# Performance work log

Hardware: AMD Instinct MI355X
Metric: run time of the kernel (lower is better)

## Reference

```python
import jax, jax.numpy as jnp
import numpy as np

N = 50000        # nodes
DEG = 16         # avg degree
E_RAND = N * DEG # random directed edges (before self-loops)
B = 4
F_IN = 64
F_OUT = 64


def _build_normalized_adjacency():
    """COO form of A_hat = D^{-1/2} (A + I) D^{-1/2} for a random sparse graph."""
    rng = np.random.default_rng(0)
    src = rng.integers(0, N, size=E_RAND)
    dst = rng.integers(0, N, size=E_RAND)
    rows = np.concatenate([src, np.arange(N)])  # add self-loops (A + I)
    cols = np.concatenate([dst, np.arange(N)])
    d = np.bincount(rows, minlength=N).astype(np.float32)  # row sums of A_tilde
    d_inv_sqrt = np.where(d > 0, 1.0 / np.sqrt(d), 0.0).astype(np.float32)
    vals = d_inv_sqrt[rows] * d_inv_sqrt[cols]
    return rows.astype(np.int32), cols.astype(np.int32), vals


def setup_inputs() -> dict:
    key = jax.random.key(0)
    k1, k2 = jax.random.split(key, 2)
    rows, cols, vals = _build_normalized_adjacency()
    x = jax.random.normal(k1, (B, N, F_IN), dtype=jnp.float32)
    # trunc_normal_(std=0.1) approximated by scaled normal
    weight = jax.random.normal(k2, (F_IN, F_OUT), dtype=jnp.float32) * 0.1
    bias = jnp.full((F_OUT,), 0.1, dtype=jnp.float32)
    return {
        "x": x,
        "vals": jnp.asarray(vals),
        "weight": weight,
        "bias": bias,
        "rows": jnp.asarray(rows),
        "cols": jnp.asarray(cols),
    }


def reference(x, vals, weight, bias, rows, cols):
    # SpMM: agg[b, r, f] = sum_e vals[e] * x[b, cols[e], f], scattered to rows[e]
    contrib = x[:, cols, :] * vals[None, :, None]          # [B, E, F_in]
    agg = jax.ops.segment_sum(contrib.transpose(1, 0, 2),  # [E, B, F_in]
                              rows, num_segments=N)        # [N, B, F_in]
    agg = agg.transpose(1, 0, 2)                           # [B, N, F_in]
    out = jnp.einsum('bnf,fo->bno', agg, weight) + bias    # dense GEMM + bias
    return jax.nn.elu(out)
```

## Files before the change

### kernel.cpp

```cpp
#include <hip/hip_runtime.h>
#include <math.h>

#define NNODES 50000
#define BB 4
#define FF 64
#define CAP 64

#define TROWS 64
#define GEMM_NB ((BB * NNODES) / TROWS)
#define RPB 4

typedef _Float16 f16;
typedef __attribute__((ext_vector_type(8))) _Float16 f16x8;
typedef __attribute__((ext_vector_type(4))) float f32x4;


__device__ inline unsigned short f2bf(float f) {
    unsigned u = __float_as_uint(f);
    u += 0x7fffu + ((u >> 16) & 1u);
    return (unsigned short)(u >> 16);
}

__device__ inline void bf4fma(float v, uint2 hv, float& a0, float& a1, float& a2, float& a3) {
    a0 = fmaf(v, __uint_as_float(hv.x << 16),         a0);
    a1 = fmaf(v, __uint_as_float(hv.x & 0xffff0000u), a1);
    a2 = fmaf(v, __uint_as_float(hv.y << 16),         a2);
    a3 = fmaf(v, __uint_as_float(hv.y & 0xffff0000u), a3);
}


__global__ __launch_bounds__(256) void prep_kernel(const int* __restrict__ rows,
                                                   const int* __restrict__ cols,
                                                   const float* __restrict__ vals,
                                                   int* __restrict__ cnt,
                                                   unsigned* __restrict__ edata, int ES,
                                                   int cstride,
                                                   const float* __restrict__ x,
                                                   const float* __restrict__ w,
                                                   unsigned short* __restrict__ h) {
    __shared__ f16 xs[64][72];
    __shared__ f16 wt[64][72];
    int t = threadIdx.x;
    long rowBase = (long)blockIdx.x * TROWS;

    int e = blockIdx.x * 256 + t;
    bool has_e = (e < ES);
    int r_e = 0, c_e = 0;
    float v_e = 0.f;
    if (has_e) { r_e = rows[e]; c_e = cols[e]; v_e = vals[e]; }

    #pragma unroll
    for (int i = 0; i < 4; ++i) {
        int s = t + i * 256;
        int r = s >> 4, c4 = s & 15;
        const float4* xp = (const float4*)(x + (rowBase + r) * 64 + c4 * 4);
        float4 xv;
        xv.x = __builtin_nontemporal_load(&xp->x);
        xv.y = __builtin_nontemporal_load(&xp->y);
        xv.z = __builtin_nontemporal_load(&xp->z);
        xv.w = __builtin_nontemporal_load(&xp->w);
        xs[r][c4 * 4 + 0] = (f16)xv.x;
        xs[r][c4 * 4 + 1] = (f16)xv.y;
        xs[r][c4 * 4 + 2] = (f16)xv.z;
        xs[r][c4 * 4 + 3] = (f16)xv.w;
        float4 wv = *(const float4*)(w + r * 64 + c4 * 4);
        wt[c4 * 4 + 0][r] = (f16)wv.x;
        wt[c4 * 4 + 1][r] = (f16)wv.y;
        wt[c4 * 4 + 2][r] = (f16)wv.z;
        wt[c4 * 4 + 3][r] = (f16)wv.w;
    }
    __syncthreads();

    int wid = t >> 6, l = t & 63;
    int arow = (wid << 4) + (l & 15);
    int kg   = (l >> 4) << 3;
    f16x8 aLo = *(const f16x8*)&xs[arow][kg];
    f16x8 aHi = *(const f16x8*)&xs[arow][32 + kg];
    f32x4 acc[4] = {{0.f,0.f,0.f,0.f},{0.f,0.f,0.f,0.f},{0.f,0.f,0.f,0.f},{0.f,0.f,0.f,0.f}};
    #pragma unroll
    for (int c = 0; c < 4; ++c) {
        f16x8 bLo = *(const f16x8*)&wt[c * 16 + (l & 15)][kg];
        f16x8 bHi = *(const f16x8*)&wt[c * 16 + (l & 15)][32 + kg];
        acc[c] = __builtin_amdgcn_mfma_f32_16x16x32_f16(aLo, bLo, acc[c], 0, 0, 0);
        acc[c] = __builtin_amdgcn_mfma_f32_16x16x32_f16(aHi, bHi, acc[c], 0, 0, 0);
    }

    int mloc = (l >> 4) << 2, fcol = l & 15;
    #pragma unroll
    for (int reg = 0; reg < 4; ++reg) {
        long m = rowBase + (wid << 4) + mloc + reg;
        int  b = (int)(m / NNODES);
        int  n = (int)(m - (long)b * NNODES);
        unsigned short* hp = h + ((size_t)n * BB + b) * 64 + fcol;
        #pragma unroll
        for (int c = 0; c < 4; ++c) hp[c * 16] = f2bf(acc[c][reg]);
    }

    if (has_e) {
        int pos = atomicAdd(&cnt[(size_t)r_e * cstride], 1);
        if (pos < CAP) {
            unsigned p = ((unsigned)f2bf(v_e) << 16) | (unsigned)c_e;
            edata[(size_t)r_e * CAP + pos] = p;
        }
    }
}


__global__ __launch_bounds__(256) void gather_kernel(const unsigned short* __restrict__ h,
                                                     const int* __restrict__ cnt,
                                                     const unsigned* __restrict__ edata,
                                                     const float* __restrict__ vals,
                                                     const float* __restrict__ bias,
                                                     float* __restrict__ out,
                                                     int cstride, int ES) {
    int wave = threadIdx.x >> 6;
    int lane = threadIdx.x & 63;
    int r = blockIdx.x * RPB + wave;
    if (r >= NNODES) return;
    int deg = cnt[(size_t)r * cstride];
    if (deg > CAP) deg = CAP;
    int b  = lane >> 4;
    int fq = lane & 15;
    const unsigned short* hb = h + b * 64 + fq * 4;
    unsigned my_p = 0u;
    if (lane < deg) {
        const unsigned* ep = &edata[(size_t)r * CAP + lane];
        my_p = __builtin_nontemporal_load(ep);
    }
    float vs = vals[ES + r];
    uint2 hs = *(const uint2*)(hb + (size_t)r * 256);
    float4 b4 = ((const float4*)bias)[fq];

    float a0 = 0.f, a1 = 0.f, a2 = 0.f, a3 = 0.f;
    int dg8 = (deg + 7) & ~7;
    for (int k = 0; k < dg8; k += 8) {
        unsigned p0 = __shfl(my_p, k,     64), p1 = __shfl(my_p, k + 1, 64);
        unsigned p2 = __shfl(my_p, k + 2, 64), p3 = __shfl(my_p, k + 3, 64);
        unsigned p4 = __shfl(my_p, k + 4, 64), p5 = __shfl(my_p, k + 5, 64);
        unsigned p6 = __shfl(my_p, k + 6, 64), p7 = __shfl(my_p, k + 7, 64);
        uint2 h0 = *(const uint2*)(hb + (size_t)(p0 & 0xFFFFu) * 256);
        uint2 h1 = *(const uint2*)(hb + (size_t)(p1 & 0xFFFFu) * 256);
        uint2 h2 = *(const uint2*)(hb + (size_t)(p2 & 0xFFFFu) * 256);
        uint2 h3 = *(const uint2*)(hb + (size_t)(p3 & 0xFFFFu) * 256);
        uint2 h4 = *(const uint2*)(hb + (size_t)(p4 & 0xFFFFu) * 256);
        uint2 h5 = *(const uint2*)(hb + (size_t)(p5 & 0xFFFFu) * 256);
        uint2 h6 = *(const uint2*)(hb + (size_t)(p6 & 0xFFFFu) * 256);
        uint2 h7 = *(const uint2*)(hb + (size_t)(p7 & 0xFFFFu) * 256);
        bf4fma(__uint_as_float(p0 & 0xFFFF0000u), h0, a0, a1, a2, a3);
        bf4fma(__uint_as_float(p1 & 0xFFFF0000u), h1, a0, a1, a2, a3);
        bf4fma(__uint_as_float(p2 & 0xFFFF0000u), h2, a0, a1, a2, a3);
        bf4fma(__uint_as_float(p3 & 0xFFFF0000u), h3, a0, a1, a2, a3);
        bf4fma(__uint_as_float(p4 & 0xFFFF0000u), h4, a0, a1, a2, a3);
        bf4fma(__uint_as_float(p5 & 0xFFFF0000u), h5, a0, a1, a2, a3);
        bf4fma(__uint_as_float(p6 & 0xFFFF0000u), h6, a0, a1, a2, a3);
        bf4fma(__uint_as_float(p7 & 0xFFFF0000u), h7, a0, a1, a2, a3);
    }
    bf4fma(vs, hs, a0, a1, a2, a3);
    a0 += b4.x; a1 += b4.y; a2 += b4.z; a3 += b4.w;
    a0 = a0 > 0.f ? a0 : expm1f(a0);
    a1 = a1 > 0.f ? a1 : expm1f(a1);
    a2 = a2 > 0.f ? a2 : expm1f(a2);
    a3 = a3 > 0.f ? a3 : expm1f(a3);
    float4 o = make_float4(a0, a1, a2, a3);
    *(float4*)(out + ((size_t)b * NNODES + r) * 64 + fq * 4) = o;
}


static inline size_t align256(size_t x) { return (x + 255) & ~(size_t)255; }

extern "C" void kernel_launch(void* const* d_in, const int* in_sizes, int n_in,
                              void* d_out, int out_size, void* d_ws, size_t ws_size,
                              hipStream_t stream) {
    const float* x    = (const float*)d_in[0];
    const float* vals = (const float*)d_in[1];
    const float* w    = (const float*)d_in[2];
    const float* bias = (const float*)d_in[3];
    const int*   rows = (const int*)d_in[4];
    const int*   cols = (const int*)d_in[5];
    float* out = (float*)d_out;
    const int E  = in_sizes[1];
    const int ES = E - NNODES;

    size_t h_b     = align256((size_t)BB * NNODES * FF * sizeof(unsigned short));
    size_t edata_b = align256((size_t)NNODES * CAP * sizeof(unsigned));
    int cstride = 16;
    if (h_b + edata_b + align256((size_t)NNODES * 16 * sizeof(int)) > ws_size) cstride = 1;

    char* ws = (char*)d_ws;
    size_t off = 0;
    unsigned short* h = (unsigned short*)(ws + off);  off += h_b;
    int* cnt = (int*)(ws + off);
    off += align256((size_t)NNODES * cstride * sizeof(int));
    unsigned* edata = (unsigned*)(ws + off);          off += edata_b;

    hipMemsetAsync(cnt, 0, (size_t)NNODES * cstride * sizeof(int), stream);
    prep_kernel<<<GEMM_NB, 256, 0, stream>>>(rows, cols, vals, cnt, edata, ES, cstride, x, w, h);
    gather_kernel<<<(NNODES + RPB - 1) / RPB, 256, 0, stream>>>(h, cnt, edata, vals, bias, out, cstride, ES);
}
```

Baseline: 133.2 us.

## Precompute transposed f16 weights once and load GEMM operands directly into registers

A new init kernel zeroes the count array (replacing hipMemsetAsync) and writes a transposed f16 copy of the weight matrix once. The prep kernel then drops its shared-memory staging and __syncthreads, loading x rows straight into MFMA operand registers and reading the pre-transposed weights from global memory. It also swaps the MFMA operand order so each lane holds four consecutive output features, which lets h be stored as ushort4 vectors instead of scalar shorts. In exchange, x is read with strided 32-byte per-lane accesses rather than fully coalesced rows, and weight reads now hit L2 from every block.

Measured after the change: 130.4 us. 2.1% less time.

```diff
diff --git a/kernel.cpp b/kernel.cpp
--- a/kernel.cpp
+++ b/kernel.cpp
@@ -11,6 +11,7 @@
 #define RPB 4
 
 typedef _Float16 f16;
+typedef __attribute__((ext_vector_type(4))) _Float16 f16x4;
 typedef __attribute__((ext_vector_type(8))) _Float16 f16x8;
 typedef __attribute__((ext_vector_type(4))) float f32x4;
 
@@ -26,6 +27,23 @@
     a1 = fmaf(v, __uint_as_float(hv.x & 0xffff0000u), a1);
     a2 = fmaf(v, __uint_as_float(hv.y << 16),         a2);
     a3 = fmaf(v, __uint_as_float(hv.y & 0xffff0000u), a3);
+}
+
+
+__global__ __launch_bounds__(256) void init_kernel(int* __restrict__ cnt, int n4,
+                                                   const float* __restrict__ w,
+                                                   f16* __restrict__ wt) {
+    int i = blockIdx.x * 256 + threadIdx.x;
+    if (i < n4) ((int4*)cnt)[i] = make_int4(0, 0, 0, 0);
+    if (i < 1024) {
+        int f = i >> 4, k0 = (i & 15) << 2;
+        f16x4 v;
+        v[0] = (f16)w[(k0 + 0) * 64 + f];
+        v[1] = (f16)w[(k0 + 1) * 64 + f];
+        v[2] = (f16)w[(k0 + 2) * 64 + f];
+        v[3] = (f16)w[(k0 + 3) * 64 + f];
+        *(f16x4*)(wt + f * 64 + k0) = v;
+    }
 }
 
 
@@ -36,12 +54,10 @@
                                                    unsigned* __restrict__ edata, int ES,
                                                    int cstride,
                                                    const float* __restrict__ x,
-                                                   const float* __restrict__ w,
+                                                   const f16* __restrict__ wt,
                                                    unsigned short* __restrict__ h) {
-    __shared__ f16 xs[64][72];
-    __shared__ f16 wt[64][72];
     int t = threadIdx.x;
-    long rowBase = (long)blockIdx.x * TROWS;
+    int wid = t >> 6, l = t & 63;
 
     int e = blockIdx.x * 256 + t;
     bool has_e = (e < ES);
@@ -49,51 +65,49 @@
     float v_e = 0.f;
     if (has_e) { r_e = rows[e]; c_e = cols[e]; v_e = vals[e]; }
 
-    #pragma unroll
-    for (int i = 0; i < 4; ++i) {
-        int s = t + i * 256;
-        int r = s >> 4, c4 = s & 15;
-        const float4* xp = (const float4*)(x + (rowBase + r) * 64 + c4 * 4);
-        float4 xv;
-        xv.x = __builtin_nontemporal_load(&xp->x);
-        xv.y = __builtin_nontemporal_load(&xp->y);
-        xv.z = __builtin_nontemporal_load(&xp->z);
-        xv.w = __builtin_nontemporal_load(&xp->w);
-        xs[r][c4 * 4 + 0] = (f16)xv.x;
-        xs[r][c4 * 4 + 1] = (f16)xv.y;
-        xs[r][c4 * 4 + 2] = (f16)xv.z;
-        xs[r][c4 * 4 + 3] = (f16)xv.w;
-        float4 wv = *(const float4*)(w + r * 64 + c4 * 4);
-        wt[c4 * 4 + 0][r] = (f16)wv.x;
-        wt[c4 * 4 + 1][r] = (f16)wv.y;
-        wt[c4 * 4 + 2][r] = (f16)wv.z;
-        wt[c4 * 4 + 3][r] = (f16)wv.w;
-    }
-    __syncthreads();
-
-    int wid = t >> 6, l = t & 63;
-    int arow = (wid << 4) + (l & 15);
-    int kg   = (l >> 4) << 3;
-    f16x8 aLo = *(const f16x8*)&xs[arow][kg];
-    f16x8 aHi = *(const f16x8*)&xs[arow][32 + kg];
+    long mcol = (long)blockIdx.x * TROWS + (wid << 4) + (l & 15);
+    int  kg   = (l >> 4) << 3;
+    const float* xp = x + mcol * 64 + kg;
+    float4 lo0, lo1, hi0, hi1;
+    {
+        const float4* p;
+        p = (const float4*)(xp);
+        lo0.x = __builtin_nontemporal_load(&p->x); lo0.y = __builtin_nontemporal_load(&p->y);
+        lo0.z = __builtin_nontemporal_load(&p->z); lo0.w = __builtin_nontemporal_load(&p->w);
+        p = (const float4*)(xp + 4);
+        lo1.x = __builtin_nontemporal_load(&p->x); lo1.y = __builtin_nontemporal_load(&p->y);
+        lo1.z = __builtin_nontemporal_load(&p->z); lo1.w = __builtin_nontemporal_load(&p->w);
+        p = (const float4*)(xp + 32);
+        hi0.x = __builtin_nontemporal_load(&p->x); hi0.y = __builtin_nontemporal_load(&p->y);
+        hi0.z = __builtin_nontemporal_load(&p->z); hi0.w = __builtin_nontemporal_load(&p->w);
+        p = (const float4*)(xp + 36);
+        hi1.x = __builtin_nontemporal_load(&p->x); hi1.y = __builtin_nontemporal_load(&p->y);
+        hi1.z = __builtin_nontemporal_load(&p->z); hi1.w = __builtin_nontemporal_load(&p->w);
+    }
+    f16x8 aLo, aHi;
+    aLo[0] = (f16)lo0.x; aLo[1] = (f16)lo0.y; aLo[2] = (f16)lo0.z; aLo[3] = (f16)lo0.w;
+    aLo[4] = (f16)lo1.x; aLo[5] = (f16)lo1.y; aLo[6] = (f16)lo1.z; aLo[7] = (f16)lo1.w;
+    aHi[0] = (f16)hi0.x; aHi[1] = (f16)hi0.y; aHi[2] = (f16)hi0.z; aHi[3] = (f16)hi0.w;
+    aHi[4] = (f16)hi1.x; aHi[5] = (f16)hi1.y; aHi[6] = (f16)hi1.z; aHi[7] = (f16)hi1.w;
+
     f32x4 acc[4] = {{0.f,0.f,0.f,0.f},{0.f,0.f,0.f,0.f},{0.f,0.f,0.f,0.f},{0.f,0.f,0.f,0.f}};
     #pragma unroll
     for (int c = 0; c < 4; ++c) {
-        f16x8 bLo = *(const f16x8*)&wt[c * 16 + (l & 15)][kg];
-        f16x8 bHi = *(const f16x8*)&wt[c * 16 + (l & 15)][32 + kg];
-        acc[c] = __builtin_amdgcn_mfma_f32_16x16x32_f16(aLo, bLo, acc[c], 0, 0, 0);
-        acc[c] = __builtin_amdgcn_mfma_f32_16x16x32_f16(aHi, bHi, acc[c], 0, 0, 0);
-    }
-
-    int mloc = (l >> 4) << 2, fcol = l & 15;
+        f16x8 bLo = *(const f16x8*)(wt + (c * 16 + (l & 15)) * 64 + kg);
+        f16x8 bHi = *(const f16x8*)(wt + (c * 16 + (l & 15)) * 64 + 32 + kg);
+        acc[c] = __builtin_amdgcn_mfma_f32_16x16x32_f16(bLo, aLo, acc[c], 0, 0, 0);
+        acc[c] = __builtin_amdgcn_mfma_f32_16x16x32_f16(bHi, aHi, acc[c], 0, 0, 0);
+    }
+
+    int b = (int)(mcol / NNODES);
+    int n = (int)(mcol - (long)b * NNODES);
+    unsigned short* hp = h + ((size_t)n * BB + b) * 64 + ((l >> 4) << 2);
     #pragma unroll
-    for (int reg = 0; reg < 4; ++reg) {
-        long m = rowBase + (wid << 4) + mloc + reg;
-        int  b = (int)(m / NNODES);
-        int  n = (int)(m - (long)b * NNODES);
-        unsigned short* hp = h + ((size_t)n * BB + b) * 64 + fcol;
-        #pragma unroll
-        for (int c = 0; c < 4; ++c) hp[c * 16] = f2bf(acc[c][reg]);
+    for (int c = 0; c < 4; ++c) {
+        ushort4 o;
+        o.x = f2bf(acc[c][0]); o.y = f2bf(acc[c][1]);
+        o.z = f2bf(acc[c][2]); o.w = f2bf(acc[c][3]);
+        *(ushort4*)(hp + c * 16) = o;
     }
 
     if (has_e) {
@@ -183,8 +197,9 @@
 
     size_t h_b     = align256((size_t)BB * NNODES * FF * sizeof(unsigned short));
     size_t edata_b = align256((size_t)NNODES * CAP * sizeof(unsigned));
+    size_t wt_b    = align256((size_t)64 * 64 * sizeof(f16));
     int cstride = 16;
-    if (h_b + edata_b + align256((size_t)NNODES * 16 * sizeof(int)) > ws_size) cstride = 1;
+    if (h_b + edata_b + wt_b + align256((size_t)NNODES * 16 * sizeof(int)) > ws_size) cstride = 1;
 
     char* ws = (char*)d_ws;
     size_t off = 0;
@@ -192,8 +207,11 @@
     int* cnt = (int*)(ws + off);
     off += align256((size_t)NNODES * cstride * sizeof(int));
     unsigned* edata = (unsigned*)(ws + off);          off += edata_b;
-
-    hipMemsetAsync(cnt, 0, (size_t)NNODES * cstride * sizeof(int), stream);
-    prep_kernel<<<GEMM_NB, 256, 0, stream>>>(rows, cols, vals, cnt, edata, ES, cstride, x, w, h);
+    f16* wt = (f16*)(ws + off);                       off += wt_b;
+
+    int n4 = (NNODES * cstride) / 4;
+
+    init_kernel<<<(n4 + 255) / 256, 256, 0, stream>>>(cnt, n4, w, wt);
+    prep_kernel<<<GEMM_NB, 256, 0, stream>>>(rows, cols, vals, cnt, edata, ES, cstride, x, wt, h);
     gather_kernel<<<(NNODES + RPB - 1) / RPB, 256, 0, stream>>>(h, cnt, edata, vals, bias, out, cstride, ES);
 }
```
